# Kernel tuning notes

Hardware: AMD Instinct MI355X
Metric: run time of the kernel (lower is better)

The kernel has to match this reference:

```python
import jax, jax.numpy as jnp
import numpy as np

KV_POOL = 2


def setup_inputs() -> dict:
    key = jax.random.key(0)
    ks = jax.random.split(key, 12)
    B, C1, C2, H, W, D = 8, 256, 512, 64, 64, 64
    s = 0.02
    return {
        "x1": jax.random.normal(ks[0], (B, C1, H, W), jnp.float32),
        "x2": jax.random.normal(ks[1], (B, C2, H, W), jnp.float32),
        "Wq": jax.random.normal(ks[2], (D, C1), jnp.float32) * s,
        "bq": jnp.zeros((D,), jnp.float32),
        "Wk": jax.random.normal(ks[3], (D, C2), jnp.float32) * s,
        "bk": jnp.zeros((D,), jnp.float32),
        "Wv": jax.random.normal(ks[4], (D, C2), jnp.float32) * s,
        "bv": jnp.zeros((D,), jnp.float32),
        "Wo": jax.random.normal(ks[5], (C1, D), jnp.float32) * s,
        "bo": jnp.zeros((C1,), jnp.float32),
    }


def reference(x1, x2, Wq, bq, Wk, bk, Wv, bv, Wo, bo):
    B, C1, H, W = x1.shape
    D = Wq.shape[0]
    # adaptive_avg_pool2d to (H//2, W//2) with even dims == 2x2 mean pool
    Bs, C2, H2, W2 = x2.shape
    x2p = x2.reshape(Bs, C2, H2 // KV_POOL, KV_POOL, W2 // KV_POOL, KV_POOL).mean(axis=(3, 5))
    # 1x1 convs as channel matmuls; flatten spatial dims
    Q = jnp.einsum('bchw,dc->bhwd', x1, Wq).reshape(B, H * W, D) + bq          # [B,N,D]
    K = jnp.einsum('bchw,dc->bhwd', x2p, Wk).reshape(B, -1, D) + bk            # [B,M,D]
    V = jnp.einsum('bchw,dc->bhwd', x2p, Wv).reshape(B, -1, D) + bv            # [B,M,D]
    attn = jax.nn.softmax(jnp.einsum('bnd,bmd->bnm', Q, K), axis=-1)           # [B,N,M]
    out = jnp.einsum('bnm,bmd->bnd', attn, V)                                  # [B,N,D]
    y = jnp.einsum('bnd,cd->bnc', out, Wo) + bo                                # [B,N,C1]
    y = y.reshape(B, H, W, C1).transpose(0, 3, 1, 2)                           # [B,C1,H,W]
    return x1 + y
```

## Files before the change

kernel.cpp:

```cpp
#include <hip/hip_runtime.h>
#include <hip/hip_bf16.h>

typedef __bf16 bf16x4 __attribute__((ext_vector_type(4)));
typedef __bf16 bf16x8 __attribute__((ext_vector_type(8)));
typedef float f32x16 __attribute__((ext_vector_type(16)));
typedef unsigned int u32x4 __attribute__((ext_vector_type(4)));

static constexpr int Bc = 8, C1 = 256, C2 = 512, Hh = 64, Ww = 64, Dd = 64;
static constexpr int Nn = 4096, Mm = 1024;

#define MFMA __builtin_amdgcn_mfma_f32_32x32x16_bf16

__device__ __forceinline__ uint32_t pkbf(float a, float b) {
  union { __bf16 h[2]; uint32_t u; } x;
  x.h[0] = (__bf16)a; x.h[1] = (__bf16)b;
  return x.u;
}

__device__ __forceinline__ bf16x8 cvt8(const float* __restrict__ p) {
  float4 a = *(const float4*)p;
  float4 b2 = *(const float4*)(p + 4);
  bf16x8 r;
  r[0] = (__bf16)a.x; r[1] = (__bf16)a.y; r[2] = (__bf16)a.z; r[3] = (__bf16)a.w;
  r[4] = (__bf16)b2.x; r[5] = (__bf16)b2.y; r[6] = (__bf16)b2.z; r[7] = (__bf16)b2.w;
  return r;
}

__device__ __forceinline__ void pack16(const float* p, bf16x8& f0, bf16x8& f1) {
  uint32_t w01 = pkbf(p[0], p[1]),   w23 = pkbf(p[2], p[3]);
  uint32_t w45 = pkbf(p[4], p[5]),   w67 = pkbf(p[6], p[7]);
  uint32_t w89 = pkbf(p[8], p[9]),   wab = pkbf(p[10], p[11]);
  uint32_t wcd = pkbf(p[12], p[13]), wef = pkbf(p[14], p[15]);
  auto s0 = __builtin_amdgcn_permlane32_swap(w01, w45, false, false);
  auto s1 = __builtin_amdgcn_permlane32_swap(w23, w67, false, false);
  auto s2 = __builtin_amdgcn_permlane32_swap(w89, wcd, false, false);
  auto s3 = __builtin_amdgcn_permlane32_swap(wab, wef, false, false);
  u32x4 q0 = {s0[0], s1[0], s0[1], s1[1]};
  u32x4 q1 = {s2[0], s3[0], s2[1], s3[1]};
  f0 = __builtin_bit_cast(bf16x8, q0);
  f1 = __builtin_bit_cast(bf16x8, q1);
}


__global__ __launch_bounds__(256) void k_proj(
    const float* __restrict__ x1, const float* __restrict__ x2,
    const float* __restrict__ Wq, const float* __restrict__ bq,
    const float* __restrict__ Wk, const float* __restrict__ bk,
    const float* __restrict__ Wv, const float* __restrict__ bv,
    __bf16* __restrict__ qfb, __bf16* __restrict__ kfb,
    __bf16* __restrict__ vfb) {
  __shared__ __align__(16) __bf16 lds[32 * 520 + 64 * 40];
  const int bx = blockIdx.x, b = blockIdx.y, tid = threadIdx.x;
  const int w = tid >> 6, l = tid & 63, h = l >> 5, nl = l & 31;

  if (bx < 64) {
    const int n0 = bx * 64;
#pragma unroll 4
    for (int it = 0; it < 64; ++it) {
      int c = it * 4 + (tid >> 6);
      int j = tid & 63;
      lds[j * 264 + c] = (__bf16)x1[(size_t)(b * C1 + c) * Nn + n0 + j];
    }
    __syncthreads();
    const int nsub = w & 1, dh = w >> 1;
    const __bf16* arow = lds + (nsub * 32 + nl) * 264;
    const float* wrow = Wq + (size_t)(dh * 32 + nl) * C1 + 8 * h;
    f32x16 acc = {};
#pragma unroll
    for (int ks = 0; ks < 16; ++ks) {
      bf16x8 a = *(const bf16x8*)(arow + ks * 16 + 8 * h);
      bf16x8 bb = cvt8(wrow + ks * 16);
      acc = MFMA(a, bb, acc, 0, 0, 0);
    }
    const int d = dh * 32 + nl;
    const float bias = bq[d];
    __bf16* qdst = qfb + (size_t)b * Nn * Dd + (size_t)((n0 >> 5) + nsub) * 2048 +
                   (d >> 4) * 512 + ((d >> 3) & 1) * 256 + (d & 7);
#pragma unroll
    for (int r = 0; r < 16; ++r) {
      int mrow = (r & 3) + 8 * (r >> 2) + 4 * h;
      qdst[mrow * 8] = (__bf16)(acc[r] + bias);
    }
  } else {
    const int h2 = bx - 64;
    __bf16* klds = lds;
    __bf16* vlds = lds + 32 * 520;
#pragma unroll 4
    for (int it = 0; it < 64; ++it) {
      int c = it * 8 + (tid >> 5);
      int j = tid & 31;
      const float* p = x2 + ((size_t)(b * C2 + c) * Hh + 2 * h2) * Ww + 2 * j;
      float2 v0 = *(const float2*)p;
      float2 v1 = *(const float2*)(p + Ww);
      klds[j * 520 + c] = (__bf16)((v0.x + v0.y + v1.x + v1.y) * 0.25f);
    }
    __syncthreads();
    const int isv = w >> 1, dh = w & 1;
    const __bf16* arow = klds + nl * 520;
    const float* wrow = (isv ? Wv : Wk) + (size_t)(dh * 32 + nl) * C2 + 8 * h;
    f32x16 acc = {};
#pragma unroll
    for (int ks = 0; ks < 32; ++ks) {
      bf16x8 a = *(const bf16x8*)(arow + ks * 16 + 8 * h);
      bf16x8 bb = cvt8(wrow + ks * 16);
      acc = MFMA(a, bb, acc, 0, 0, 0);
    }
    const int d = dh * 32 + nl;
    const float bias = isv ? bv[d] : bk[d];
    if (!isv) {
      __bf16* kdst = kfb + (size_t)b * Mm * Dd + (size_t)h2 * 2048 +
                     (d >> 4) * 512 + ((d >> 3) & 1) * 256 + (d & 7);
#pragma unroll
      for (int r = 0; r < 16; ++r) {
        int mr = (r & 3) + 8 * (r >> 2) + 4 * h;
        kdst[mr * 8] = (__bf16)(acc[r] + bias);
      }
    } else {
#pragma unroll
      for (int r = 0; r < 16; ++r) {
        int mr = (r & 3) + 8 * (r >> 2) + 4 * h;
        vlds[d * 40 + mr] = (__bf16)(acc[r] + bias);
      }
    }
    __syncthreads();
    const int dd = tid >> 2, q = tid & 3;
    bf16x8 vv = *(const bf16x8*)(vlds + dd * 40 + q * 8);
    const int c = (q >> 1) * 2 + (dd >> 5);
    const int ll = (q & 1) * 32 + (dd & 31);
    *(bf16x8*)(vfb + (size_t)b * Mm * Dd + (size_t)h2 * 2048 + c * 512 + ll * 8) = vv;
  }
}

template <int S>
__global__ __launch_bounds__(256) void k_attn_part(
    const __bf16* __restrict__ qfb, const __bf16* __restrict__ kfb,
    const __bf16* __restrict__ vfb, __bf16* __restrict__ po,
    float* __restrict__ pml) {
  const int lin = blockIdx.x;
  const int b = lin & 7, rest = lin >> 3, nblk = rest & 31, sp = rest >> 5;
  const int tid = threadIdx.x;
  const int w = tid >> 6, l = tid & 63, h = l >> 5, nl = l & 31;
  const int n = nblk * 128 + w * 32 + nl;
  constexpr int NT = Mm / S / 32;
  const int t0 = sp * NT;

  const __bf16* qt = qfb + (size_t)b * Nn * Dd + (size_t)(nblk * 4 + w) * 2048 + l * 8;
  bf16x8 qf0 = *(const bf16x8*)(qt);
  bf16x8 qf1 = *(const bf16x8*)(qt + 512);
  bf16x8 qf2 = *(const bf16x8*)(qt + 1024);
  bf16x8 qf3 = *(const bf16x8*)(qt + 1536);

  const __bf16* kt = kfb + (size_t)b * Mm * Dd + (size_t)t0 * 2048 + l * 8;
  const __bf16* vt = vfb + (size_t)b * Mm * Dd + (size_t)t0 * 2048 + l * 8;

  f32x16 o0 = {}, o1 = {};
  float lsum = 0.f;

  bf16x8 ck0 = *(const bf16x8*)(kt);
  bf16x8 ck1 = *(const bf16x8*)(kt + 512);
  bf16x8 ck2 = *(const bf16x8*)(kt + 1024);
  bf16x8 ck3 = *(const bf16x8*)(kt + 1536);
  bf16x8 cv0 = *(const bf16x8*)(vt);
  bf16x8 cv1 = *(const bf16x8*)(vt + 512);
  bf16x8 cv2 = *(const bf16x8*)(vt + 1024);
  bf16x8 cv3 = *(const bf16x8*)(vt + 1536);

#pragma unroll
  for (int i = 0; i < NT; ++i) {
    bf16x8 nk0, nk1, nk2, nk3, nv0, nv1, nv2, nv3;
    if (i + 1 < NT) {
      const __bf16* kn = kt + (size_t)(i + 1) * 2048;
      const __bf16* vn = vt + (size_t)(i + 1) * 2048;
      nk0 = *(const bf16x8*)(kn);
      nk1 = *(const bf16x8*)(kn + 512);
      nk2 = *(const bf16x8*)(kn + 1024);
      nk3 = *(const bf16x8*)(kn + 1536);
      nv0 = *(const bf16x8*)(vn);
      nv1 = *(const bf16x8*)(vn + 512);
      nv2 = *(const bf16x8*)(vn + 1024);
      nv3 = *(const bf16x8*)(vn + 1536);
    }
    f32x16 s = {};
    s = MFMA(ck0, qf0, s, 0, 0, 0);
    s = MFMA(ck1, qf1, s, 0, 0, 0);
    s = MFMA(ck2, qf2, s, 0, 0, 0);
    s = MFMA(ck3, qf3, s, 0, 0, 0);
    float p[16];
#pragma unroll
    for (int r = 0; r < 16; ++r) p[r] = __expf(s[r]);
    float u0 = (p[0] + p[1]) + (p[2] + p[3]);
    float u1 = (p[4] + p[5]) + (p[6] + p[7]);
    float u2 = (p[8] + p[9]) + (p[10] + p[11]);
    float u3 = (p[12] + p[13]) + (p[14] + p[15]);
    lsum += (u0 + u1) + (u2 + u3);
    bf16x8 pb0, pb1;
    pack16(p, pb0, pb1);
    o0 = MFMA(cv0, pb0, o0, 0, 0, 0);
    o1 = MFMA(cv1, pb0, o1, 0, 0, 0);
    o0 = MFMA(cv2, pb1, o0, 0, 0, 0);
    o1 = MFMA(cv3, pb1, o1, 0, 0, 0);
    if (i + 1 < NT) {
      ck0 = nk0; ck1 = nk1; ck2 = nk2; ck3 = nk3;
      cv0 = nv0; cv1 = nv1; cv2 = nv2; cv3 = nv3;
    }
  }

  const float ltot = lsum + __shfl_xor(lsum, 32);
  __bf16* ob = po + (size_t)(b * S + sp) * 16 * Nn * 4 + (size_t)n * 4;
#pragma unroll
  for (int q = 0; q < 4; ++q) {
    bf16x4 t0v, t1v;
#pragma unroll
    for (int e = 0; e < 4; ++e) {
      t0v[e] = (__bf16)o0[q * 4 + e];
      t1v[e] = (__bf16)o1[q * 4 + e];
    }
    *(bf16x4*)(ob + (size_t)(2 * q + h) * Nn * 4) = t0v;
    *(bf16x4*)(ob + (size_t)(8 + 2 * q + h) * Nn * 4) = t1v;
  }
  if (h == 0) pml[(size_t)(b * S + sp) * Nn + n] = ltot;
}

template <int S>
__global__ __launch_bounds__(256) void k_attn_comb(
    const float* __restrict__ x1, const __bf16* __restrict__ po,
    const float* __restrict__ pml, const float* __restrict__ Wo,
    const float* __restrict__ bo, float* __restrict__ out) {
  const int lin = blockIdx.x;
  const int b = lin & 7, rest = lin >> 3, nblk = rest & 31, ctg = rest >> 5;
  const int tid = threadIdx.x;
  const int w = tid >> 6, l = tid & 63, h = l >> 5, nl = l & 31;
  const int n = nblk * 128 + w * 32 + nl;

  float L = 0.f;
#pragma unroll
  for (int s = 0; s < S; ++s)
    L += pml[(size_t)(b * S + s) * Nn + n];
  const float inv = 1.f / L;

  float o[32];
#pragma unroll
  for (int r = 0; r < 32; ++r) o[r] = 0.f;
#pragma unroll
  for (int s = 0; s < S; ++s) {
    const __bf16* ob = po + (size_t)(b * S + s) * 16 * Nn * 4 + (size_t)n * 4;
#pragma unroll
    for (int q = 0; q < 4; ++q) {
      bf16x4 v0 = *(const bf16x4*)(ob + (size_t)(2 * q + h) * Nn * 4);
      bf16x4 v1 = *(const bf16x4*)(ob + (size_t)(8 + 2 * q + h) * Nn * 4);
#pragma unroll
      for (int e = 0; e < 4; ++e) {
        o[q * 4 + e] += (float)v0[e];
        o[16 + q * 4 + e] += (float)v1[e];
      }
    }
  }

  bf16x8 obf[4];
#pragma unroll
  for (int a2 = 0; a2 < 2; ++a2) {
    float ov[16];
#pragma unroll
    for (int r = 0; r < 16; ++r) ov[r] = o[a2 * 16 + r] * inv;
    pack16(ov, obf[a2 * 2], obf[a2 * 2 + 1]);
  }

  const float* x1r = x1 + (size_t)b * C1 * Nn + n;
  float* outr = out + (size_t)b * C1 * Nn + n;
  const float* wobase = Wo + (size_t)nl * Dd + 8 * h;
#pragma unroll
  for (int ci = 0; ci < 4; ++ci) {
    const int ct = ctg * 4 + ci;
    f32x16 y = {};
    const float* wr = wobase + (size_t)ct * 32 * Dd;
#pragma unroll
    for (int ks = 0; ks < 4; ++ks) {
      bf16x8 a = cvt8(wr + ks * 16);
      y = MFMA(a, obf[ks], y, 0, 0, 0);
    }
#pragma unroll
    for (int r = 0; r < 16; ++r) {
      int c = ct * 32 + (r & 3) + 8 * (r >> 2) + 4 * h;
      size_t idx = (size_t)c * Nn;
      outr[idx] = y[r] + bo[c] + x1r[idx];
    }
  }
}

__global__ __launch_bounds__(256) void k_attn(
    const float* __restrict__ x1, const __bf16* __restrict__ qfb,
    const __bf16* __restrict__ kfb, const __bf16* __restrict__ vfb,
    const float* __restrict__ Wo, const float* __restrict__ bo,
    float* __restrict__ out) {
  const int b = blockIdx.y, tid = threadIdx.x;
  const int w = tid >> 6, l = tid & 63, h = l >> 5, nl = l & 31;
  const int n = blockIdx.x * 128 + w * 32 + nl;

  const __bf16* qt = qfb + (size_t)b * Nn * Dd + (size_t)(blockIdx.x * 4 + w) * 2048 + l * 8;
  bf16x8 qf0 = *(const bf16x8*)(qt);
  bf16x8 qf1 = *(const bf16x8*)(qt + 512);
  bf16x8 qf2 = *(const bf16x8*)(qt + 1024);
  bf16x8 qf3 = *(const bf16x8*)(qt + 1536);

  f32x16 o0 = {}, o1 = {};
  float mrun = -INFINITY, lsum = 0.f;

  const __bf16* kb_ = kfb + (size_t)b * Mm * Dd + l * 8;
  const __bf16* vb_ = vfb + (size_t)b * Mm * Dd + l * 8;

  for (int t = 0; t < 32; ++t) {
    const __bf16* kt = kb_ + (size_t)t * 2048;
    const __bf16* vt = vb_ + (size_t)t * 2048;
    bf16x8 ka0 = *(const bf16x8*)(kt);
    bf16x8 ka1 = *(const bf16x8*)(kt + 512);
    bf16x8 ka2 = *(const bf16x8*)(kt + 1024);
    bf16x8 ka3 = *(const bf16x8*)(kt + 1536);
    bf16x8 v00 = *(const bf16x8*)(vt);
    bf16x8 v10 = *(const bf16x8*)(vt + 512);
    bf16x8 v01 = *(const bf16x8*)(vt + 1024);
    bf16x8 v11 = *(const bf16x8*)(vt + 1536);
    f32x16 s = {};
    s = MFMA(ka0, qf0, s, 0, 0, 0);
    s = MFMA(ka1, qf1, s, 0, 0, 0);
    s = MFMA(ka2, qf2, s, 0, 0, 0);
    s = MFMA(ka3, qf3, s, 0, 0, 0);
    float tmax = s[0];
#pragma unroll
    for (int r = 1; r < 16; ++r) tmax = fmaxf(tmax, s[r]);
    tmax = fmaxf(tmax, __shfl_xor(tmax, 32));
    const float mnew = fmaxf(mrun, tmax);
    const float scale = __expf(mrun - mnew);
    float p[16], psum = 0.f;
#pragma unroll
    for (int r = 0; r < 16; ++r) { p[r] = __expf(s[r] - mnew); psum += p[r]; }
    lsum = lsum * scale + psum;
    mrun = mnew;
#pragma unroll
    for (int r = 0; r < 16; ++r) { o0[r] *= scale; o1[r] *= scale; }
    bf16x8 pb0, pb1;
    pack16(p, pb0, pb1);
    o0 = MFMA(v00, pb0, o0, 0, 0, 0);
    o1 = MFMA(v10, pb0, o1, 0, 0, 0);
    o0 = MFMA(v01, pb1, o0, 0, 0, 0);
    o1 = MFMA(v11, pb1, o1, 0, 0, 0);
  }

  const float ltot = lsum + __shfl_xor(lsum, 32);
  const float inv = 1.f / ltot;

  bf16x8 ob[4];
#pragma unroll
  for (int a2 = 0; a2 < 2; ++a2) {
    float ov[16];
#pragma unroll
    for (int r = 0; r < 16; ++r) ov[r] = (a2 ? o1[r] : o0[r]) * inv;
    pack16(ov, ob[a2 * 2], ob[a2 * 2 + 1]);
  }

  const float* x1r = x1 + (size_t)b * C1 * Nn + n;
  float* outr = out + (size_t)b * C1 * Nn + n;
  const float* wobase = Wo + (size_t)nl * Dd + 8 * h;
#pragma unroll 2
  for (int ct = 0; ct < 8; ++ct) {
    f32x16 y = {};
    const float* wr = wobase + (size_t)ct * 32 * Dd;
#pragma unroll
    for (int ks = 0; ks < 4; ++ks) {
      bf16x8 a = cvt8(wr + ks * 16);
      y = MFMA(a, ob[ks], y, 0, 0, 0);
    }
#pragma unroll
    for (int r = 0; r < 16; ++r) {
      int c = ct * 32 + (r & 3) + 8 * (r >> 2) + 4 * h;
      size_t idx = (size_t)c * Nn;
      outr[idx] = y[r] + bo[c] + x1r[idx];
    }
  }
}

extern "C" void kernel_launch(void* const* d_in, const int* in_sizes, int n_in,
                              void* d_out, int out_size, void* d_ws,
                              size_t ws_size, hipStream_t stream) {
  const float* x1 = (const float*)d_in[0];
  const float* x2 = (const float*)d_in[1];
  const float* Wq = (const float*)d_in[2];
  const float* bq = (const float*)d_in[3];
  const float* Wk = (const float*)d_in[4];
  const float* bk = (const float*)d_in[5];
  const float* Wv = (const float*)d_in[6];
  const float* bv = (const float*)d_in[7];
  const float* Wo = (const float*)d_in[8];
  const float* bo = (const float*)d_in[9];
  float* out = (float*)d_out;
  char* ws = (char*)d_ws;

  __bf16* qfb = (__bf16*)(ws);
  __bf16* kfb = (__bf16*)(ws + 4194304);
  __bf16* vfb = (__bf16*)(ws + 5242880);
  __bf16* po  = (__bf16*)(ws + 6291456);
  const size_t ws8 = 6291456ull + 33554432ull + 1048576ull;
  const size_t ws4 = 6291456ull + 16777216ull + 524288ull;

  hipLaunchKernelGGL(k_proj, dim3(96, 8), dim3(256), 0, stream,
                     x1, x2, Wq, bq, Wk, bk, Wv, bv, qfb, kfb, vfb);
  if (ws_size >= ws8) {
    float* pml = (float*)(ws + 6291456 + 33554432);
    hipLaunchKernelGGL(k_attn_part<8>, dim3(32 * 8 * 8), dim3(256), 0, stream,
                       qfb, kfb, vfb, po, pml);
    hipLaunchKernelGGL(k_attn_comb<8>, dim3(32 * 8 * 2), dim3(256), 0, stream,
                       x1, po, pml, Wo, bo, out);
  } else if (ws_size >= ws4) {
    float* pml = (float*)(ws + 6291456 + 16777216);
    hipLaunchKernelGGL(k_attn_part<4>, dim3(32 * 8 * 4), dim3(256), 0, stream,
                       qfb, kfb, vfb, po, pml);
    hipLaunchKernelGGL(k_attn_comb<4>, dim3(32 * 8 * 2), dim3(256), 0, stream,
                       x1, po, pml, Wo, bo, out);
  } else {
    hipLaunchKernelGGL(k_attn, dim3(32, 8), dim3(256), 0, stream,
                       x1, qfb, kfb, vfb, Wo, bo, out);
  }
}
```

Before: 72.21 us.

## Pre-convert weights to bf16 MFMA fragment layout and vectorize x1 loads

Adds a small kernel that converts Wq, Wk, Wv and Wo once per call into bf16, pre-swizzled into MFMA operand order, so the projection and output kernels load one bf16x8 per step instead of converting fp32 weights each time. The x1 staging loop now uses float4 loads, and the LDS row pitches change from 264/520/40 to 266/522/42, likely to reduce bank conflicts. The cost is an extra kernel launch and a slightly larger workspace.

```diff
diff --git a/kernel.cpp b/kernel.cpp
--- a/kernel.cpp
+++ b/kernel.cpp
@@ -41,35 +41,70 @@
   f1 = __builtin_bit_cast(bf16x8, q1);
 }
 
+__global__ __launch_bounds__(256) void k_prep_w(
+    const float* __restrict__ Wq, const float* __restrict__ Wk,
+    const float* __restrict__ Wv, const float* __restrict__ Wo,
+    __bf16* __restrict__ wqf, __bf16* __restrict__ wkf,
+    __bf16* __restrict__ wvf, __bf16* __restrict__ wof) {
+  int t = blockIdx.x * 256 + threadIdx.x;
+  if (t < 2048) {
+    int l = t & 63, g = t >> 6;
+    int dh = g >> 4, ks = g & 15;
+    int d = dh * 32 + (l & 31), c = ks * 16 + (l >> 5) * 8;
+    *(bf16x8*)(wqf + (size_t)t * 8) = cvt8(Wq + (size_t)d * C1 + c);
+  } else if (t < 6144) {
+    int tt = t - 2048;
+    int l = tt & 63, g = tt >> 6;
+    int dh = g >> 5, ks = g & 31;
+    int d = dh * 32 + (l & 31), c = ks * 16 + (l >> 5) * 8;
+    *(bf16x8*)(wkf + (size_t)tt * 8) = cvt8(Wk + (size_t)d * C2 + c);
+  } else if (t < 10240) {
+    int tt = t - 6144;
+    int l = tt & 63, g = tt >> 6;
+    int dh = g >> 5, ks = g & 31;
+    int d = dh * 32 + (l & 31), c = ks * 16 + (l >> 5) * 8;
+    *(bf16x8*)(wvf + (size_t)tt * 8) = cvt8(Wv + (size_t)d * C2 + c);
+  } else if (t < 12288) {
+    int tt = t - 10240;
+    int l = tt & 63, g = tt >> 6;
+    int ct = g >> 2, ks = g & 3;
+    int crow = ct * 32 + (l & 31), d = ks * 16 + (l >> 5) * 8;
+    *(bf16x8*)(wof + (size_t)tt * 8) = cvt8(Wo + (size_t)crow * Dd + d);
+  }
+}
 
 __global__ __launch_bounds__(256) void k_proj(
     const float* __restrict__ x1, const float* __restrict__ x2,
-    const float* __restrict__ Wq, const float* __restrict__ bq,
-    const float* __restrict__ Wk, const float* __restrict__ bk,
-    const float* __restrict__ Wv, const float* __restrict__ bv,
+    const __bf16* __restrict__ wqf, const float* __restrict__ bq,
+    const __bf16* __restrict__ wkf, const float* __restrict__ bk,
+    const __bf16* __restrict__ wvf, const float* __restrict__ bv,
     __bf16* __restrict__ qfb, __bf16* __restrict__ kfb,
     __bf16* __restrict__ vfb) {
-  __shared__ __align__(16) __bf16 lds[32 * 520 + 64 * 40];
+  __shared__ __align__(16) __bf16 lds[19392];
   const int bx = blockIdx.x, b = blockIdx.y, tid = threadIdx.x;
   const int w = tid >> 6, l = tid & 63, h = l >> 5, nl = l & 31;
 
   if (bx < 64) {
     const int n0 = bx * 64;
 #pragma unroll 4
-    for (int it = 0; it < 64; ++it) {
-      int c = it * 4 + (tid >> 6);
-      int j = tid & 63;
-      lds[j * 264 + c] = (__bf16)x1[(size_t)(b * C1 + c) * Nn + n0 + j];
+    for (int it = 0; it < 16; ++it) {
+      int c = it * 16 + (tid >> 4);
+      int q = tid & 15;
+      float4 v = *(const float4*)(x1 + (size_t)(b * C1 + c) * Nn + n0 + 4 * q);
+      lds[(4 * q + 0) * 266 + c] = (__bf16)v.x;
+      lds[(4 * q + 1) * 266 + c] = (__bf16)v.y;
+      lds[(4 * q + 2) * 266 + c] = (__bf16)v.z;
+      lds[(4 * q + 3) * 266 + c] = (__bf16)v.w;
     }
     __syncthreads();
     const int nsub = w & 1, dh = w >> 1;
-    const __bf16* arow = lds + (nsub * 32 + nl) * 264;
-    const float* wrow = Wq + (size_t)(dh * 32 + nl) * C1 + 8 * h;
+    const __bf16* arow = lds + (nsub * 32 + nl) * 266;
+    const __bf16* wq8 = wqf + (size_t)dh * 16 * 512 + l * 8;
     f32x16 acc = {};
 #pragma unroll
     for (int ks = 0; ks < 16; ++ks) {
       bf16x8 a = *(const bf16x8*)(arow + ks * 16 + 8 * h);
-      bf16x8 bb = cvt8(wrow + ks * 16);
+      bf16x8 bb = *(const bf16x8*)(wq8 + ks * 512);
       acc = MFMA(a, bb, acc, 0, 0, 0);
     }
     const int d = dh * 32 + nl;
@@ -84,7 +119,7 @@
   } else {
     const int h2 = bx - 64;
     __bf16* klds = lds;
-    __bf16* vlds = lds + 32 * 520;
+    __bf16* vlds = lds + 32 * 522;
 #pragma unroll 4
     for (int it = 0; it < 64; ++it) {
       int c = it * 8 + (tid >> 5);
@@ -92,17 +127,17 @@
       const float* p = x2 + ((size_t)(b * C2 + c) * Hh + 2 * h2) * Ww + 2 * j;
       float2 v0 = *(const float2*)p;
       float2 v1 = *(const float2*)(p + Ww);
-      klds[j * 520 + c] = (__bf16)((v0.x + v0.y + v1.x + v1.y) * 0.25f);
+      klds[j * 522 + c] = (__bf16)((v0.x + v0.y + v1.x + v1.y) * 0.25f);
     }
     __syncthreads();
     const int isv = w >> 1, dh = w & 1;
-    const __bf16* arow = klds + nl * 520;
-    const float* wrow = (isv ? Wv : Wk) + (size_t)(dh * 32 + nl) * C2 + 8 * h;
+    const __bf16* arow = klds + nl * 522;
+    const __bf16* wf8 = (isv ? wvf : wkf) + (size_t)dh * 32 * 512 + l * 8;
     f32x16 acc = {};
 #pragma unroll
     for (int ks = 0; ks < 32; ++ks) {
       bf16x8 a = *(const bf16x8*)(arow + ks * 16 + 8 * h);
-      bf16x8 bb = cvt8(wrow + ks * 16);
+      bf16x8 bb = *(const bf16x8*)(wf8 + ks * 512);
       acc = MFMA(a, bb, acc, 0, 0, 0);
     }
     const int d = dh * 32 + nl;
@@ -119,12 +154,12 @@
 #pragma unroll
       for (int r = 0; r < 16; ++r) {
         int mr = (r & 3) + 8 * (r >> 2) + 4 * h;
-        vlds[d * 40 + mr] = (__bf16)(acc[r] + bias);
+        vlds[d * 42 + mr] = (__bf16)(acc[r] + bias);
       }
     }
     __syncthreads();
     const int dd = tid >> 2, q = tid & 3;
-    bf16x8 vv = *(const bf16x8*)(vlds + dd * 40 + q * 8);
+    bf16x8 vv = *(const bf16x8*)(vlds + dd * 42 + q * 8);
     const int c = (q >> 1) * 2 + (dd >> 5);
     const int ll = (q & 1) * 32 + (dd & 31);
     *(bf16x8*)(vfb + (size_t)b * Mm * Dd + (size_t)h2 * 2048 + c * 512 + ll * 8) = vv;
@@ -224,7 +259,7 @@
 template <int S>
 __global__ __launch_bounds__(256) void k_attn_comb(
     const float* __restrict__ x1, const __bf16* __restrict__ po,
-    const float* __restrict__ pml, const float* __restrict__ Wo,
+    const float* __restrict__ pml, const __bf16* __restrict__ wof,
     const float* __restrict__ bo, float* __restrict__ out) {
   const int lin = blockIdx.x;
   const int b = lin & 7, rest = lin >> 3, nblk = rest & 31, ctg = rest >> 5;
@@ -267,15 +302,13 @@
 
   const float* x1r = x1 + (size_t)b * C1 * Nn + n;
   float* outr = out + (size_t)b * C1 * Nn + n;
-  const float* wobase = Wo + (size_t)nl * Dd + 8 * h;
 #pragma unroll
   for (int ci = 0; ci < 4; ++ci) {
     const int ct = ctg * 4 + ci;
     f32x16 y = {};
-    const float* wr = wobase + (size_t)ct * 32 * Dd;
 #pragma unroll
     for (int ks = 0; ks < 4; ++ks) {
-      bf16x8 a = cvt8(wr + ks * 16);
+      bf16x8 a = *(const bf16x8*)(wof + (size_t)((ct * 4 + ks) * 64 + l) * 8);
       y = MFMA(a, obf[ks], y, 0, 0, 0);
     }
 #pragma unroll
@@ -290,7 +323,7 @@
 __global__ __launch_bounds__(256) void k_attn(
     const float* __restrict__ x1, const __bf16* __restrict__ qfb,
     const __bf16* __restrict__ kfb, const __bf16* __restrict__ vfb,
-    const float* __restrict__ Wo, const float* __restrict__ bo,
+    const __bf16* __restrict__ wof, const float* __restrict__ bo,
     float* __restrict__ out) {
   const int b = blockIdx.y, tid = threadIdx.x;
   const int w = tid >> 6, l = tid & 63, h = l >> 5, nl = l & 31;
@@ -359,14 +392,12 @@
 
   const float* x1r = x1 + (size_t)b * C1 * Nn + n;
   float* outr = out + (size_t)b * C1 * Nn + n;
-  const float* wobase = Wo + (size_t)nl * Dd + 8 * h;
 #pragma unroll 2
   for (int ct = 0; ct < 8; ++ct) {
     f32x16 y = {};
-    const float* wr = wobase + (size_t)ct * 32 * Dd;
 #pragma unroll
     for (int ks = 0; ks < 4; ++ks) {
-      bf16x8 a = cvt8(wr + ks * 16);
+      bf16x8 a = *(const bf16x8*)(wof + (size_t)((ct * 4 + ks) * 64 + l) * 8);
       y = MFMA(a, ob[ks], y, 0, 0, 0);
     }
 #pragma unroll
@@ -394,29 +425,35 @@
   float* out = (float*)d_out;
   char* ws = (char*)d_ws;
 
-  __bf16* qfb = (__bf16*)(ws);
-  __bf16* kfb = (__bf16*)(ws + 4194304);
-  __bf16* vfb = (__bf16*)(ws + 5242880);
-  __bf16* po  = (__bf16*)(ws + 6291456);
-  const size_t ws8 = 6291456ull + 33554432ull + 1048576ull;
-  const size_t ws4 = 6291456ull + 16777216ull + 524288ull;
-
+  __bf16* wqf = (__bf16*)(ws);
+  __bf16* wkf = (__bf16*)(ws + 32768);
+  __bf16* wvf = (__bf16*)(ws + 98304);
+  __bf16* wof = (__bf16*)(ws + 163840);
+  __bf16* qfb = (__bf16*)(ws + 196608);
+  __bf16* kfb = (__bf16*)(ws + 4390912);
+  __bf16* vfb = (__bf16*)(ws + 5439488);
+  __bf16* po  = (__bf16*)(ws + 6488064);
+  const size_t ws8 = 6488064ull + 33554432ull + 1048576ull;
+  const size_t ws4 = 6488064ull + 16777216ull + 524288ull;
+
+  hipLaunchKernelGGL(k_prep_w, dim3(48), dim3(256), 0, stream,
+                     Wq, Wk, Wv, Wo, wqf, wkf, wvf, wof);
   hipLaunchKernelGGL(k_proj, dim3(96, 8), dim3(256), 0, stream,
-                     x1, x2, Wq, bq, Wk, bk, Wv, bv, qfb, kfb, vfb);
+                     x1, x2, wqf, bq, wkf, bk, wvf, bv, qfb, kfb, vfb);
   if (ws_size >= ws8) {
-    float* pml = (float*)(ws + 6291456 + 33554432);
+    float* pml = (float*)(ws + 6488064 + 33554432);
     hipLaunchKernelGGL(k_attn_part<8>, dim3(32 * 8 * 8), dim3(256), 0, stream,
                        qfb, kfb, vfb, po, pml);
     hipLaunchKernelGGL(k_attn_comb<8>, dim3(32 * 8 * 2), dim3(256), 0, stream,
-                       x1, po, pml, Wo, bo, out);
+                       x1, po, pml, wof, bo, out);
   } else if (ws_size >= ws4) {
-    float* pml = (float*)(ws + 6291456 + 16777216);
+    float* pml = (float*)(ws + 6488064 + 16777216);
     hipLaunchKernelGGL(k_attn_part<4>, dim3(32 * 8 * 4), dim3(256), 0, stream,
                        qfb, kfb, vfb, po, pml);
     hipLaunchKernelGGL(k_attn_comb<4>, dim3(32 * 8 * 2), dim3(256), 0, stream,
-                       x1, po, pml, Wo, bo, out);
+                       x1, po, pml, wof, bo, out);
   } else {
     hipLaunchKernelGGL(k_attn, dim3(32, 8), dim3(256), 0, stream,
-                       x1, qfb, kfb, vfb, Wo, bo, out);
-  }
-}
+                       x1, qfb, kfb, vfb, wof, bo, out);
+  }
+}
```

New measurement: 63.36 us. 12.2% less time.
